# Optimization experiments

Hardware: AMD Instinct MI355X
Metric: run time of the kernel (lower is better)

Reference implementation:

```python
import jax, jax.numpy as jnp
import numpy as np

TAU = 0.5
EPS = 1e-12  # F.normalize default eps


def _projection(z, fc1_w, fc1_b, fc2_w, fc2_b):
    h = jax.nn.elu(z @ fc1_w.T + fc1_b)
    return h @ fc2_w.T + fc2_b


def _normalize(z):
    n = jnp.linalg.norm(z, axis=1, keepdims=True)
    return z / jnp.maximum(n, EPS)


def _semi_loss(h1, h2):
    z1 = _normalize(h1)
    z2 = _normalize(h2)
    refl_sim = jnp.exp((z1 @ z1.T) / TAU)      # [N, N]
    between_sim = jnp.exp((z1 @ z2.T) / TAU)   # [N, N]
    pos = jnp.diagonal(between_sim)
    denom = refl_sim.sum(axis=1) + between_sim.sum(axis=1) - jnp.diagonal(refl_sim)
    return -jnp.log(pos / denom)


def setup_inputs() -> dict:
    key = jax.random.key(0)
    k1, k2, k3, k4 = jax.random.split(key, 4)
    N, H, P = 8192, 512, 512
    s1 = 1.0 / np.sqrt(H)
    s2 = 1.0 / np.sqrt(P)
    return {
        "z1": jax.random.normal(k1, (N, H), jnp.float32),
        "z2": jax.random.normal(k2, (N, H), jnp.float32),
        "fc1_w": jax.random.normal(k3, (P, H), jnp.float32) * s1,
        "fc1_b": jnp.zeros((P,), jnp.float32),
        "fc2_w": jax.random.normal(k4, (H, P), jnp.float32) * s2,
        "fc2_b": jnp.zeros((H,), jnp.float32),
    }


def reference(z1, z2, fc1_w, fc1_b, fc2_w, fc2_b):
    h1 = _projection(z1, fc1_w, fc1_b, fc2_w, fc2_b)
    h2 = _projection(z2, fc1_w, fc1_b, fc2_w, fc2_b)
    l1 = _semi_loss(h1, h2)
    l2 = _semi_loss(h2, h1)
    ret = (l1 + l2) * 0.5
    return ret.mean()
```

## Files before the change

### kernel.cpp

```cpp
#include <hip/hip_runtime.h>
#include <math.h>

typedef __attribute__((ext_vector_type(8))) __bf16 bf16x8;
typedef __attribute__((ext_vector_type(4))) float f32x4;
typedef __attribute__((ext_vector_type(16))) float f32x16;
typedef __attribute__((ext_vector_type(8))) unsigned short u16x8;
typedef __attribute__((ext_vector_type(8))) int i32x8;

#define GAS(p) ((const __attribute__((address_space(1))) void*)(p))
#define LAS(p) ((__attribute__((address_space(3))) void*)(p))

__device__ __forceinline__ unsigned short f2bf(float f) {
  union { float f; unsigned int u; } v; v.f = f;
  unsigned int r = (v.u + 0x7FFFu + ((v.u >> 16) & 1u)) >> 16;
  return (unsigned short)r;
}
__device__ __forceinline__ float bf2f(unsigned short b) {
  union { unsigned int u; float f; } v; v.u = ((unsigned int)b) << 16;
  return v.f;
}

__global__ __launch_bounds__(256) void cast_all_kernel(
    const float* __restrict__ z1, const float* __restrict__ z2,
    const float* __restrict__ w1, const float* __restrict__ w2,
    unsigned short* __restrict__ z1b, unsigned short* __restrict__ z2b,
    unsigned short* __restrict__ w1b, unsigned short* __restrict__ w2b) {
  int b = blockIdx.x;
  const float* in; unsigned short* out; int base;
  if (b < 4096)       { in = z1; out = z1b; base = b; }
  else if (b < 8192)  { in = z2; out = z2b; base = b - 4096; }
  else if (b < 8448)  { in = w1; out = w1b; base = b - 8192; }
  else                { in = w2; out = w2b; base = b - 8448; }
  int i = (base * 256 + threadIdx.x) * 4;
  float4 v = *(const float4*)(in + i);
  ushort4 o;
  o.x = f2bf(v.x); o.y = f2bf(v.y); o.z = f2bf(v.z); o.w = f2bf(v.w);
  *(ushort4*)(out + i) = o;
}

__device__ __forceinline__ void gemm_tile_512(
    const unsigned short* __restrict__ A, const unsigned short* __restrict__ B,
    int m0, int n0, unsigned short* lA, unsigned short* lB, f32x4 acc[4][4]) {
  constexpr int K = 512;
  const int tid  = threadIdx.x;
  const int wave = tid >> 6;
  const int lane = tid & 63;
  const int quad = lane >> 4;
  const int l16  = lane & 15;
  const int wrow = (wave & 1) * 64;
  const int wcol = (wave >> 1) * 64;

  const f32x4 zero = {0.f, 0.f, 0.f, 0.f};
#pragma unroll
  for (int i = 0; i < 4; ++i)
#pragma unroll
    for (int j = 0; j < 4; ++j) acc[i][j] = zero;

  const int e0 = wave * 1024 + lane * 8;
  const int r0 = e0 >> 5, c0 = e0 & 31;
  const int e1 = e0 + 512;
  const int r1 = e1 >> 5, c1 = e1 & 31;

  const unsigned short* Ag0 = A + (size_t)(m0 + r0) * K + c0;
  const unsigned short* Ag1 = A + (size_t)(m0 + r1) * K + c1;
  const unsigned short* Bg0 = B + (size_t)(n0 + r0) * K + c0;
  const unsigned short* Bg1 = B + (size_t)(n0 + r1) * K + c1;

  for (int kt = 0; kt < K; kt += 32) {
    __syncthreads();
    __builtin_amdgcn_global_load_lds(GAS(Ag0 + kt), LAS(&lA[e0]), 16, 0, 0);
    __builtin_amdgcn_global_load_lds(GAS(Ag1 + kt), LAS(&lA[e1]), 16, 0, 0);
    __builtin_amdgcn_global_load_lds(GAS(Bg0 + kt), LAS(&lB[e0]), 16, 0, 0);
    __builtin_amdgcn_global_load_lds(GAS(Bg1 + kt), LAS(&lB[e1]), 16, 0, 0);
    __syncthreads();

    bf16x8 af[4], bfr[4];
#pragma unroll
    for (int i = 0; i < 4; ++i) {
      af[i]  = *(const bf16x8*)&lA[(wrow + i * 16 + l16) * 32 + quad * 8];
      bfr[i] = *(const bf16x8*)&lB[(wcol + i * 16 + l16) * 32 + quad * 8];
    }
#pragma unroll
    for (int mi = 0; mi < 4; ++mi)
#pragma unroll
      for (int ni = 0; ni < 4; ++ni)
        acc[mi][ni] = __builtin_amdgcn_mfma_f32_16x16x32_bf16(
            af[mi], bfr[ni], acc[mi][ni], 0, 0, 0);
  }
}

template<int EPI>
__global__ __launch_bounds__(256)
void proj_kernel(const unsigned short* __restrict__ A1,
                 const unsigned short* __restrict__ A2,
                 const unsigned short* __restrict__ W,
                 const float* __restrict__ bias,
                 unsigned short* __restrict__ C1,
                 unsigned short* __restrict__ C2) {
  __shared__ unsigned short lA[128 * 32];
  __shared__ unsigned short lB[128 * 32];
  const int b = blockIdx.x;
  const int which = b >> 8;
  const int r = b & 255;
  const int n0 = (r & 3) * 128;
  const int m0 = (r >> 2) * 128;
  const unsigned short* A = which ? A2 : A1;
  unsigned short* C = which ? C2 : C1;

  f32x4 acc[4][4];
  gemm_tile_512(A, W, m0, n0, lA, lB, acc);

  const int lane = threadIdx.x & 63;
  const int wave = threadIdx.x >> 6;
  const int quad = lane >> 4;
  const int l16  = lane & 15;
  const int wrow = (wave & 1) * 64;
  const int wcol = (wave >> 1) * 64;

#pragma unroll
  for (int ni = 0; ni < 4; ++ni) {
    const int c = n0 + wcol + ni * 16 + l16;
    const float bv = bias[c];
#pragma unroll
    for (int mi = 0; mi < 4; ++mi) {
      const int rbase = m0 + wrow + mi * 16 + quad * 4;
#pragma unroll
      for (int rr = 0; rr < 4; ++rr) {
        float v = acc[mi][ni][rr] + bv;
        if constexpr (EPI == 0) v = (v > 0.f) ? v : expm1f(v);
        C[(size_t)(rbase + rr) * 512 + c] = f2bf(v);
      }
    }
  }
}

__global__ __launch_bounds__(256, 2)
void gram_kernel(const unsigned char* __restrict__ q1,
                 const unsigned char* __restrict__ q2,
                 float* __restrict__ d11, float* __restrict__ d22,
                 float* __restrict__ d12r, float* __restrict__ d12c) {
  __shared__ unsigned char lA[65536];

  const int b = blockIdx.x;
  const unsigned char *Abase, *Bbase;
  float *rptr, *cptr;
  int by, g, cnt;
  bool cross;
  if (b < 1088) {
    const bool first = (b < 544);
    int j = first ? b : b - 544;
    int q = (int)((sqrtf(2.f * j + 1.f) - 1.f) * 0.5f);
    while (2 * (q + 1) * (q + 2) <= j) ++q;
    while (2 * q * (q + 1) > j) --q;
    const int w = j - 2 * q * (q + 1);
    const int dr = w / (q + 1);
    g = w - dr * (q + 1);
    by = 4 * q + dr;
    const unsigned char* h = first ? q1 : q2;
    Abase = h; Bbase = h;
    rptr = first ? d11 : d22; cptr = rptr;
    cnt = min(4, by + 1 - g * 4);
    cross = false;
  } else {
    const int j = b - 1088;
    g = j >> 6; by = j & 63;
    Abase = q1; Bbase = q2;
    rptr = d12r; cptr = d12c;
    cnt = 4; cross = true;
  }

  const int tid  = threadIdx.x;
  const int wave = tid >> 6;
  const int lane = tid & 63;
  const int half = lane >> 5;
  const int l31  = lane & 31;
  const int pa0 = (wave & 1) * 2;
  const int pb0 = (wave >> 1) * 2;
  const int lfo = half * 1024 + l31 * 16;

  {
    const unsigned char* Asrc = Abase + (size_t)(by * 4 + wave) * 16384 + lane * 16;
    unsigned char* Adst = lA + wave * 16384 + lane * 16;
#pragma unroll
    for (int i = 0; i < 16; ++i)
      __builtin_amdgcn_global_load_lds(GAS(Asrc + i * 1024),
                                       LAS(Adst + i * 1024), 16, 0, 0);
  }
  __syncthreads();

  union frag { i32x8 v; int4 h[2]; };

  float rs[2][16];
#pragma unroll
  for (int mi = 0; mi < 2; ++mi)
#pragma unroll
    for (int rr = 0; rr < 16; ++rr) rs[mi][rr] = 0.f;

  for (int t = 0; t < cnt; ++t) {
    const int ct = g * 4 + t;
    const unsigned char* B0 = Bbase + (size_t)(ct * 4 + pb0) * 16384 + lfo;
    const unsigned char* B1 = B0 + 16384;

    f32x16 acc[2][2];
#pragma unroll
    for (int i = 0; i < 2; ++i)
#pragma unroll
      for (int jj = 0; jj < 2; ++jj)
#pragma unroll
        for (int rr = 0; rr < 16; ++rr) acc[i][jj][rr] = 0.f;

#pragma unroll
    for (int KT = 0; KT < 4; ++KT) {
#pragma unroll
      for (int ktl = 0; ktl < 2; ++ktl) {
        const int ko = KT * 4096 + ktl * 2048;
        frag fa[2], fb[2];
        fb[0].h[0] = *(const int4*)(B0 + ko);
        fb[0].h[1] = *(const int4*)(B0 + ko + 512);
        fb[1].h[0] = *(const int4*)(B1 + ko);
        fb[1].h[1] = *(const int4*)(B1 + ko + 512);
#pragma unroll
        for (int i = 0; i < 2; ++i) {
          const int oa = (pa0 + i) * 16384 + ko + lfo;
          fa[i].h[0] = *(const int4*)&lA[oa];
          fa[i].h[1] = *(const int4*)&lA[oa + 512];
        }
#pragma unroll
        for (int mi = 0; mi < 2; ++mi)
#pragma unroll
          for (int ni = 0; ni < 2; ++ni)
            acc[mi][ni] = __builtin_amdgcn_mfma_scale_f32_32x32x64_f8f6f4(
                fa[mi].v, fb[ni].v, acc[mi][ni],
                0, 0,
                0, 0x7F7F7F7F,
                0, 0x7F7F7F7F);
      }
    }

    float cs[2] = {0.f, 0.f};
#pragma unroll
    for (int mi = 0; mi < 2; ++mi)
#pragma unroll
      for (int ni = 0; ni < 2; ++ni)
#pragma unroll
        for (int rr = 0; rr < 16; ++rr) {
          float v = __expf(2.0f * acc[mi][ni][rr]);
          rs[mi][rr] += v;
          cs[ni] += v;
        }
    const bool diag = (!cross) && (ct == by);
    if (!diag) {
#pragma unroll
      for (int ni = 0; ni < 2; ++ni) {
        float v = cs[ni] + __shfl_xor(cs[ni], 32, 64);
        if (half == 0)
          atomicAdd(&cptr[ct * 128 + (wave >> 1) * 64 + ni * 32 + l31], v);
      }
    }
  }

#pragma unroll
  for (int mi = 0; mi < 2; ++mi) {
#pragma unroll
    for (int d = 1; d < 32; d <<= 1) {
#pragma unroll
      for (int rr = 0; rr < 16; ++rr) rs[mi][rr] += __shfl_xor(rs[mi][rr], d, 64);
    }
    if (l31 == 0) {
      const int mb = by * 128 + (wave & 1) * 64 + mi * 32;
#pragma unroll
      for (int rr = 0; rr < 16; ++rr) {
        const int row = mb + (rr & 3) + 8 * (rr >> 2) + 4 * half;
        atomicAdd(&rptr[row], rs[mi][rr]);
      }
    }
  }
}

__global__ __launch_bounds__(256)
void norm_diag_kernel(const unsigned short* __restrict__ h1,
                      const unsigned short* __restrict__ h2,
                      unsigned char* __restrict__ q1,
                      unsigned char* __restrict__ q2,
                      float* __restrict__ cdiag) {
  const int wave = threadIdx.x >> 6, lane = threadIdx.x & 63;
  const int row = blockIdx.x * 4 + wave;
  const u16x8 u1 = *(const u16x8*)(h1 + (size_t)row * 512 + lane * 8);
  const u16x8 u2 = *(const u16x8*)(h2 + (size_t)row * 512 + lane * 8);
  float f1[8], f2[8], ss1 = 0.f, ss2 = 0.f;
#pragma unroll
  for (int j = 0; j < 8; ++j) {
    f1[j] = bf2f(u1[j]); ss1 += f1[j] * f1[j];
    f2[j] = bf2f(u2[j]); ss2 += f2[j] * f2[j];
  }
#pragma unroll
  for (int d = 1; d < 64; d <<= 1) {
    ss1 += __shfl_xor(ss1, d, 64);
    ss2 += __shfl_xor(ss2, d, 64);
  }
  const float inv1 = 1.0f / fmaxf(sqrtf(ss1), 1e-12f);
  const float inv2 = 1.0f / fmaxf(sqrtf(ss2), 1e-12f);
  float a[8], bb[8];
  float dot = 0.f;
#pragma unroll
  for (int j = 0; j < 8; ++j) {
    a[j] = f1[j] * inv1; bb[j] = f2[j] * inv2;
    dot += a[j] * bb[j];
  }
  int lo1 = __builtin_amdgcn_cvt_pk_fp8_f32(a[0], a[1], 0, false);
  lo1 = __builtin_amdgcn_cvt_pk_fp8_f32(a[2], a[3], lo1, true);
  int hi1 = __builtin_amdgcn_cvt_pk_fp8_f32(a[4], a[5], 0, false);
  hi1 = __builtin_amdgcn_cvt_pk_fp8_f32(a[6], a[7], hi1, true);
  int lo2 = __builtin_amdgcn_cvt_pk_fp8_f32(bb[0], bb[1], 0, false);
  lo2 = __builtin_amdgcn_cvt_pk_fp8_f32(bb[2], bb[3], lo2, true);
  int hi2 = __builtin_amdgcn_cvt_pk_fp8_f32(bb[4], bb[5], 0, false);
  hi2 = __builtin_amdgcn_cvt_pk_fp8_f32(bb[6], bb[7], hi2, true);

  const int c0 = lane * 8;
  const size_t dst = (size_t)(row >> 5) * 16384 + (c0 >> 6) * 2048
                   + ((c0 >> 4) & 3) * 512 + (row & 31) * 16 + (c0 & 15);
  *(int2*)(q1 + dst) = make_int2(lo1, hi1);
  *(int2*)(q2 + dst) = make_int2(lo2, hi2);
#pragma unroll
  for (int d = 1; d < 64; d <<= 1) dot += __shfl_xor(dot, d, 64);
  if (lane == 0) cdiag[row] = dot;
}

__global__ __launch_bounds__(256)
void finalize_kernel(const float* __restrict__ d11, const float* __restrict__ d22,
                     const float* __restrict__ d12r, const float* __restrict__ d12c,
                     const float* __restrict__ cdiag, float* __restrict__ out) {
  const float e2 = 7.38905609893065f;
  float s = 0.f;
  for (int i = threadIdx.x; i < 8192; i += 256) {
    const float den1 = d11[i] + d12r[i] - e2;
    const float den2 = d22[i] + d12c[i] - e2;
    s += -2.0f * cdiag[i] + 0.5f * (logf(den1) + logf(den2));
  }
#pragma unroll
  for (int d = 1; d < 64; d <<= 1) s += __shfl_xor(s, d, 64);
  __shared__ float sm[4];
  if ((threadIdx.x & 63) == 0) sm[threadIdx.x >> 6] = s;
  __syncthreads();
  if (threadIdx.x == 0) out[0] = (sm[0] + sm[1] + sm[2] + sm[3]) * (1.0f / 8192.0f);
}

extern "C" void kernel_launch(void* const* d_in, const int* in_sizes, int n_in,
                              void* d_out, int out_size, void* d_ws, size_t ws_size,
                              hipStream_t stream) {
  const float* z1 = (const float*)d_in[0];
  const float* z2 = (const float*)d_in[1];
  const float* w1 = (const float*)d_in[2];
  const float* b1 = (const float*)d_in[3];
  const float* w2 = (const float*)d_in[4];
  const float* b2 = (const float*)d_in[5];
  float* out = (float*)d_out;

  const int N = 8192, D = 512;
  char* ws = (char*)d_ws;
  auto alloc = [&](size_t bytes) {
    char* p = ws; ws += (bytes + 255) & ~(size_t)255; return p;
  };
  unsigned short* z1b = (unsigned short*)alloc((size_t)N * D * 2);
  unsigned short* z2b = (unsigned short*)alloc((size_t)N * D * 2);
  unsigned short* g1  = (unsigned short*)alloc((size_t)N * D * 2);
  unsigned short* g2  = (unsigned short*)alloc((size_t)N * D * 2);
  unsigned short* w1b = (unsigned short*)alloc((size_t)D * D * 2);
  unsigned short* w2b = (unsigned short*)alloc((size_t)D * D * 2);
  float* sums  = (float*)alloc((size_t)4 * N * sizeof(float));
  float* cdiag = (float*)alloc((size_t)N * sizeof(float));
  float* d11 = sums, *d22 = sums + N, *d12r = sums + 2 * N, *d12c = sums + 3 * N;
  unsigned short* h1 = z1b;
  unsigned short* h2 = z2b;
  unsigned char* q1 = (unsigned char*)g1;
  unsigned char* q2 = (unsigned char*)g2;

  hipMemsetAsync(sums, 0, (size_t)4 * N * sizeof(float), stream);

  cast_all_kernel<<<dim3(8704), 256, 0, stream>>>(z1, z2, w1, w2, z1b, z2b, w1b, w2b);
  proj_kernel<0><<<dim3(512), 256, 0, stream>>>(z1b, z2b, w1b, b1, g1, g2);
  proj_kernel<1><<<dim3(512), 256, 0, stream>>>(g1, g2, w2b, b2, h1, h2);
  norm_diag_kernel<<<dim3(N / 4), 256, 0, stream>>>(h1, h2, q1, q2, cdiag);
  gram_kernel<<<dim3(2112), 256, 0, stream>>>(q1, q2, d11, d22, d12r, d12c);
  finalize_kernel<<<1, 256, 0, stream>>>(d11, d22, d12r, d12c, cdiag, out);
}
```

Baseline: 246.1 us.

## Double-buffer projection GEMM LDS and retile gram kernel to 64-row blocks

The projection GEMM now double-buffers its LDS tiles, issuing the next k-slice's global-to-LDS loads before computing on the current one, with a single barrier per iteration. The gram kernel is retiled so each block holds a 64-row A strip (32 KB LDS) and each wave owns a 64-column slice of a 256-column B supertile. This doubles the number of blocks and raises the occupancy target to 4 blocks per CU. Waves skip sub-diagonal work inside diagonal supertiles, and the exponential is rewritten as exp2 with a folded constant. The risks are more atomics and duplicated B reads, plus the question of whether the single barrier per iteration is enough to order the LDS buffer reuse.

```diff
diff --git a/kernel.cpp b/kernel.cpp
--- a/kernel.cpp
+++ b/kernel.cpp
@@ -38,7 +38,7 @@
   *(ushort4*)(out + i) = o;
 }
 
-__device__ __forceinline__ void gemm_tile_512(
+__device__ __forceinline__ void gemm_tile_512_db(
     const unsigned short* __restrict__ A, const unsigned short* __restrict__ B,
     int m0, int n0, unsigned short* lA, unsigned short* lB, f32x4 acc[4][4]) {
   constexpr int K = 512;
@@ -66,19 +66,27 @@
   const unsigned short* Bg0 = B + (size_t)(n0 + r0) * K + c0;
   const unsigned short* Bg1 = B + (size_t)(n0 + r1) * K + c1;
 
-  for (int kt = 0; kt < K; kt += 32) {
-    __syncthreads();
-    __builtin_amdgcn_global_load_lds(GAS(Ag0 + kt), LAS(&lA[e0]), 16, 0, 0);
-    __builtin_amdgcn_global_load_lds(GAS(Ag1 + kt), LAS(&lA[e1]), 16, 0, 0);
-    __builtin_amdgcn_global_load_lds(GAS(Bg0 + kt), LAS(&lB[e0]), 16, 0, 0);
-    __builtin_amdgcn_global_load_lds(GAS(Bg1 + kt), LAS(&lB[e1]), 16, 0, 0);
-    __syncthreads();
-
+  __builtin_amdgcn_global_load_lds(GAS(Ag0), LAS(&lA[e0]), 16, 0, 0);
+  __builtin_amdgcn_global_load_lds(GAS(Ag1), LAS(&lA[e1]), 16, 0, 0);
+  __builtin_amdgcn_global_load_lds(GAS(Bg0), LAS(&lB[e0]), 16, 0, 0);
+  __builtin_amdgcn_global_load_lds(GAS(Bg1), LAS(&lB[e1]), 16, 0, 0);
+  __syncthreads();
+
+  for (int kt = 0; kt < 16; ++kt) {
+    const int cur = (kt & 1) * 4096;
+    if (kt < 15) {
+      const int nxt = 4096 - cur;
+      const int ko = (kt + 1) * 32;
+      __builtin_amdgcn_global_load_lds(GAS(Ag0 + ko), LAS(&lA[nxt + e0]), 16, 0, 0);
+      __builtin_amdgcn_global_load_lds(GAS(Ag1 + ko), LAS(&lA[nxt + e1]), 16, 0, 0);
+      __builtin_amdgcn_global_load_lds(GAS(Bg0 + ko), LAS(&lB[nxt + e0]), 16, 0, 0);
+      __builtin_amdgcn_global_load_lds(GAS(Bg1 + ko), LAS(&lB[nxt + e1]), 16, 0, 0);
+    }
     bf16x8 af[4], bfr[4];
 #pragma unroll
     for (int i = 0; i < 4; ++i) {
-      af[i]  = *(const bf16x8*)&lA[(wrow + i * 16 + l16) * 32 + quad * 8];
-      bfr[i] = *(const bf16x8*)&lB[(wcol + i * 16 + l16) * 32 + quad * 8];
+      af[i]  = *(const bf16x8*)&lA[cur + (wrow + i * 16 + l16) * 32 + quad * 8];
+      bfr[i] = *(const bf16x8*)&lB[cur + (wcol + i * 16 + l16) * 32 + quad * 8];
     }
 #pragma unroll
     for (int mi = 0; mi < 4; ++mi)
@@ -86,6 +94,7 @@
       for (int ni = 0; ni < 4; ++ni)
         acc[mi][ni] = __builtin_amdgcn_mfma_f32_16x16x32_bf16(
             af[mi], bfr[ni], acc[mi][ni], 0, 0, 0);
+    __syncthreads();
   }
 }
 
@@ -97,8 +106,8 @@
                  const float* __restrict__ bias,
                  unsigned short* __restrict__ C1,
                  unsigned short* __restrict__ C2) {
-  __shared__ unsigned short lA[128 * 32];
-  __shared__ unsigned short lB[128 * 32];
+  __shared__ unsigned short lA[2 * 128 * 32];
+  __shared__ unsigned short lB[2 * 128 * 32];
   const int b = blockIdx.x;
   const int which = b >> 8;
   const int r = b & 255;
@@ -108,7 +117,7 @@
   unsigned short* C = which ? C2 : C1;
 
   f32x4 acc[4][4];
-  gemm_tile_512(A, W, m0, n0, lA, lB, acc);
+  gemm_tile_512_db(A, W, m0, n0, lA, lB, acc);
 
   const int lane = threadIdx.x & 63;
   const int wave = threadIdx.x >> 6;
@@ -134,39 +143,39 @@
   }
 }
 
-__global__ __launch_bounds__(256, 2)
+__global__ __launch_bounds__(256, 4)
 void gram_kernel(const unsigned char* __restrict__ q1,
                  const unsigned char* __restrict__ q2,
                  float* __restrict__ d11, float* __restrict__ d22,
                  float* __restrict__ d12r, float* __restrict__ d12c) {
-  __shared__ unsigned char lA[65536];
+  __shared__ unsigned char lA[32768];
 
   const int b = blockIdx.x;
   const unsigned char *Abase, *Bbase;
   float *rptr, *cptr;
-  int by, g, cnt;
+  int r, g, cnt;
   bool cross;
-  if (b < 1088) {
-    const bool first = (b < 544);
-    int j = first ? b : b - 544;
-    int q = (int)((sqrtf(2.f * j + 1.f) - 1.f) * 0.5f);
-    while (2 * (q + 1) * (q + 2) <= j) ++q;
-    while (2 * q * (q + 1) > j) --q;
-    const int w = j - 2 * q * (q + 1);
-    const int dr = w / (q + 1);
-    g = w - dr * (q + 1);
-    by = 4 * q + dr;
+  if (b < 2176) {
+    const bool first = (b < 1088);
+    int j = first ? b : b - 1088;
+    int q = (int)((sqrtf((float)j + 1.f) - 1.f) * 0.5f);
+    while (4 * (q + 1) * (q + 2) <= j) ++q;
+    while (4 * q * (q + 1) > j) --q;
+    const int w = j - 4 * q * (q + 1);
+    const int s = w / (q + 1);
+    g = w - s * (q + 1);
+    r = 8 * q + s;
     const unsigned char* h = first ? q1 : q2;
     Abase = h; Bbase = h;
     rptr = first ? d11 : d22; cptr = rptr;
-    cnt = min(4, by + 1 - g * 4);
+    cnt = min(2, (r >> 2) + 1 - 2 * g);
     cross = false;
   } else {
-    const int j = b - 1088;
-    g = j >> 6; by = j & 63;
+    const int j = b - 2176;
+    g = j >> 7; r = j & 127;
     Abase = q1; Bbase = q2;
     rptr = d12r; cptr = d12c;
-    cnt = 4; cross = true;
+    cnt = 2; cross = true;
   }
 
   const int tid  = threadIdx.x;
@@ -174,15 +183,13 @@
   const int lane = tid & 63;
   const int half = lane >> 5;
   const int l31  = lane & 31;
-  const int pa0 = (wave & 1) * 2;
-  const int pb0 = (wave >> 1) * 2;
-  const int lfo = half * 1024 + l31 * 16;
+  const int lfo  = half * 1024 + l31 * 16;
 
   {
-    const unsigned char* Asrc = Abase + (size_t)(by * 4 + wave) * 16384 + lane * 16;
-    unsigned char* Adst = lA + wave * 16384 + lane * 16;
-#pragma unroll
-    for (int i = 0; i < 16; ++i)
+    const unsigned char* Asrc = Abase + (size_t)r * 32768 + wave * 8192 + lane * 16;
+    unsigned char* Adst = lA + wave * 8192 + lane * 16;
+#pragma unroll
+    for (int i = 0; i < 8; ++i)
       __builtin_amdgcn_global_load_lds(GAS(Asrc + i * 1024),
                                        LAS(Adst + i * 1024), 16, 0, 0);
   }
@@ -196,9 +203,12 @@
 #pragma unroll
     for (int rr = 0; rr < 16; ++rr) rs[mi][rr] = 0.f;
 
+  const int d = r & 3;
   for (int t = 0; t < cnt; ++t) {
-    const int ct = g * 4 + t;
-    const unsigned char* B0 = Bbase + (size_t)(ct * 4 + pb0) * 16384 + lfo;
+    const int c = 2 * g + t;
+    const bool diagST = (!cross) && (c == (r >> 2));
+    if (diagST && wave > d) break;
+    const unsigned char* B0 = Bbase + (size_t)(8 * c + 2 * wave) * 16384 + lfo;
     const unsigned char* B1 = B0 + 16384;
 
     f32x16 acc[2][2];
@@ -221,7 +231,7 @@
         fb[1].h[1] = *(const int4*)(B1 + ko + 512);
 #pragma unroll
         for (int i = 0; i < 2; ++i) {
-          const int oa = (pa0 + i) * 16384 + ko + lfo;
+          const int oa = i * 16384 + ko + lfo;
           fa[i].h[0] = *(const int4*)&lA[oa];
           fa[i].h[1] = *(const int4*)&lA[oa + 512];
         }
@@ -244,17 +254,16 @@
       for (int ni = 0; ni < 2; ++ni)
 #pragma unroll
         for (int rr = 0; rr < 16; ++rr) {
-          float v = __expf(2.0f * acc[mi][ni][rr]);
+          float v = exp2f(2.8853900817779268f * acc[mi][ni][rr]);
           rs[mi][rr] += v;
           cs[ni] += v;
         }
-    const bool diag = (!cross) && (ct == by);
-    if (!diag) {
+    if (!(diagST && wave == d)) {
 #pragma unroll
       for (int ni = 0; ni < 2; ++ni) {
         float v = cs[ni] + __shfl_xor(cs[ni], 32, 64);
         if (half == 0)
-          atomicAdd(&cptr[ct * 128 + (wave >> 1) * 64 + ni * 32 + l31], v);
+          atomicAdd(&cptr[c * 256 + wave * 64 + ni * 32 + l31], v);
       }
     }
   }
@@ -262,12 +271,12 @@
 #pragma unroll
   for (int mi = 0; mi < 2; ++mi) {
 #pragma unroll
-    for (int d = 1; d < 32; d <<= 1) {
-#pragma unroll
-      for (int rr = 0; rr < 16; ++rr) rs[mi][rr] += __shfl_xor(rs[mi][rr], d, 64);
+    for (int dd = 1; dd < 32; dd <<= 1) {
+#pragma unroll
+      for (int rr = 0; rr < 16; ++rr) rs[mi][rr] += __shfl_xor(rs[mi][rr], dd, 64);
     }
     if (l31 == 0) {
-      const int mb = by * 128 + (wave & 1) * 64 + mi * 32;
+      const int mb = r * 64 + mi * 32;
 #pragma unroll
       for (int rr = 0; rr < 16; ++rr) {
         const int row = mb + (rr & 3) + 8 * (rr >> 2) + 4 * half;
@@ -381,6 +390,6 @@
   proj_kernel<0><<<dim3(512), 256, 0, stream>>>(z1b, z2b, w1b, b1, g1, g2);
   proj_kernel<1><<<dim3(512), 256, 0, stream>>>(g1, g2, w2b, b2, h1, h2);
   norm_diag_kernel<<<dim3(N / 4), 256, 0, stream>>>(h1, h2, q1, q2, cdiag);
-  gram_kernel<<<dim3(2112), 256, 0, stream>>>(q1, q2, d11, d22, d12r, d12c);
+  gram_kernel<<<dim3(4224), 256, 0, stream>>>(q1, q2, d11, d22, d12r, d12c);
   finalize_kernel<<<1, 256, 0, stream>>>(d11, d22, d12r, d12c, cdiag, out);
 }
```

Result: slower. 299.6 us (+21.7%).

## Double-buffer projection GEMM LDS tiles and prefetch B fragments in sim kernel

Applied to the files above, without the earlier changes.

The projection GEMM now double-buffers its LDS tiles: the loads for the next K-slice are issued before computing on the current one, and one barrier per iteration replaces two. The similarity kernel keeps a 4-deep ring of B-fragment registers and prefetches two K-steps ahead, crossing into the next column tile, so global load latency overlaps the MFMA work. The exp is rewritten as exp2f with a prescaled constant. The cost is double the LDS in the projection kernel and more registers in the sim kernel, which may reduce occupancy.

```diff
diff --git a/kernel.cpp b/kernel.cpp
--- a/kernel.cpp
+++ b/kernel.cpp
@@ -38,7 +38,7 @@
   *(ushort4*)(out + i) = o;
 }
 
-__device__ __forceinline__ void gemm_tile_512(
+__device__ __forceinline__ void gemm_tile_512_db(
     const unsigned short* __restrict__ A, const unsigned short* __restrict__ B,
     int m0, int n0, unsigned short* lA, unsigned short* lB, f32x4 acc[4][4]) {
   constexpr int K = 512;
@@ -66,19 +66,27 @@
   const unsigned short* Bg0 = B + (size_t)(n0 + r0) * K + c0;
   const unsigned short* Bg1 = B + (size_t)(n0 + r1) * K + c1;
 
-  for (int kt = 0; kt < K; kt += 32) {
-    __syncthreads();
-    __builtin_amdgcn_global_load_lds(GAS(Ag0 + kt), LAS(&lA[e0]), 16, 0, 0);
-    __builtin_amdgcn_global_load_lds(GAS(Ag1 + kt), LAS(&lA[e1]), 16, 0, 0);
-    __builtin_amdgcn_global_load_lds(GAS(Bg0 + kt), LAS(&lB[e0]), 16, 0, 0);
-    __builtin_amdgcn_global_load_lds(GAS(Bg1 + kt), LAS(&lB[e1]), 16, 0, 0);
-    __syncthreads();
-
+  __builtin_amdgcn_global_load_lds(GAS(Ag0), LAS(&lA[e0]), 16, 0, 0);
+  __builtin_amdgcn_global_load_lds(GAS(Ag1), LAS(&lA[e1]), 16, 0, 0);
+  __builtin_amdgcn_global_load_lds(GAS(Bg0), LAS(&lB[e0]), 16, 0, 0);
+  __builtin_amdgcn_global_load_lds(GAS(Bg1), LAS(&lB[e1]), 16, 0, 0);
+  __syncthreads();
+
+  for (int kt = 0; kt < 16; ++kt) {
+    const int cur = (kt & 1) * 4096;
+    if (kt < 15) {
+      const int nxt = 4096 - cur;
+      const int ko = (kt + 1) * 32;
+      __builtin_amdgcn_global_load_lds(GAS(Ag0 + ko), LAS(&lA[nxt + e0]), 16, 0, 0);
+      __builtin_amdgcn_global_load_lds(GAS(Ag1 + ko), LAS(&lA[nxt + e1]), 16, 0, 0);
+      __builtin_amdgcn_global_load_lds(GAS(Bg0 + ko), LAS(&lB[nxt + e0]), 16, 0, 0);
+      __builtin_amdgcn_global_load_lds(GAS(Bg1 + ko), LAS(&lB[nxt + e1]), 16, 0, 0);
+    }
     bf16x8 af[4], bfr[4];
 #pragma unroll
     for (int i = 0; i < 4; ++i) {
-      af[i]  = *(const bf16x8*)&lA[(wrow + i * 16 + l16) * 32 + quad * 8];
-      bfr[i] = *(const bf16x8*)&lB[(wcol + i * 16 + l16) * 32 + quad * 8];
+      af[i]  = *(const bf16x8*)&lA[cur + (wrow + i * 16 + l16) * 32 + quad * 8];
+      bfr[i] = *(const bf16x8*)&lB[cur + (wcol + i * 16 + l16) * 32 + quad * 8];
     }
 #pragma unroll
     for (int mi = 0; mi < 4; ++mi)
@@ -86,6 +94,7 @@
       for (int ni = 0; ni < 4; ++ni)
         acc[mi][ni] = __builtin_amdgcn_mfma_f32_16x16x32_bf16(
             af[mi], bfr[ni], acc[mi][ni], 0, 0, 0);
+    __syncthreads();
   }
 }
 
@@ -97,8 +106,8 @@
                  const float* __restrict__ bias,
                  unsigned short* __restrict__ C1,
                  unsigned short* __restrict__ C2) {
-  __shared__ unsigned short lA[128 * 32];
-  __shared__ unsigned short lB[128 * 32];
+  __shared__ unsigned short lA[2 * 128 * 32];
+  __shared__ unsigned short lB[2 * 128 * 32];
   const int b = blockIdx.x;
   const int which = b >> 8;
   const int r = b & 255;
@@ -108,7 +117,7 @@
   unsigned short* C = which ? C2 : C1;
 
   f32x4 acc[4][4];
-  gemm_tile_512(A, W, m0, n0, lA, lB, acc);
+  gemm_tile_512_db(A, W, m0, n0, lA, lB, acc);
 
   const int lane = threadIdx.x & 63;
   const int wave = threadIdx.x >> 6;
@@ -190,16 +199,30 @@
 
   union frag { i32x8 v; int4 h[2]; };
 
+  auto LDB = [&](frag* dst, const unsigned char* base, int uu) {
+    const int off = (uu >> 1) * 4096 + (uu & 1) * 2048;
+    dst[0].h[0] = *(const int4*)(base + off);
+    dst[0].h[1] = *(const int4*)(base + off + 512);
+    dst[1].h[0] = *(const int4*)(base + 16384 + off);
+    dst[1].h[1] = *(const int4*)(base + 16384 + off + 512);
+  };
+
   float rs[2][16];
 #pragma unroll
   for (int mi = 0; mi < 2; ++mi)
 #pragma unroll
     for (int rr = 0; rr < 16; ++rr) rs[mi][rr] = 0.f;
+
+  frag fb[4][2];
+  const unsigned char* curB =
+      Bbase + (size_t)(g * 4 * 4 + pb0) * 16384 + lfo;
+  LDB(fb[0], curB, 0);
+  LDB(fb[1], curB, 1);
 
   for (int t = 0; t < cnt; ++t) {
     const int ct = g * 4 + t;
-    const unsigned char* B0 = Bbase + (size_t)(ct * 4 + pb0) * 16384 + lfo;
-    const unsigned char* B1 = B0 + 16384;
+    const unsigned char* nxtB = curB + 4 * 16384;
+    const bool hasNext = (t + 1 < cnt);
 
     f32x16 acc[2][2];
 #pragma unroll
@@ -210,31 +233,27 @@
         for (int rr = 0; rr < 16; ++rr) acc[i][jj][rr] = 0.f;
 
 #pragma unroll
-    for (int KT = 0; KT < 4; ++KT) {
-#pragma unroll
-      for (int ktl = 0; ktl < 2; ++ktl) {
-        const int ko = KT * 4096 + ktl * 2048;
-        frag fa[2], fb[2];
-        fb[0].h[0] = *(const int4*)(B0 + ko);
-        fb[0].h[1] = *(const int4*)(B0 + ko + 512);
-        fb[1].h[0] = *(const int4*)(B1 + ko);
-        fb[1].h[1] = *(const int4*)(B1 + ko + 512);
-#pragma unroll
-        for (int i = 0; i < 2; ++i) {
-          const int oa = (pa0 + i) * 16384 + ko + lfo;
-          fa[i].h[0] = *(const int4*)&lA[oa];
-          fa[i].h[1] = *(const int4*)&lA[oa + 512];
-        }
-#pragma unroll
-        for (int mi = 0; mi < 2; ++mi)
-#pragma unroll
-          for (int ni = 0; ni < 2; ++ni)
-            acc[mi][ni] = __builtin_amdgcn_mfma_scale_f32_32x32x64_f8f6f4(
-                fa[mi].v, fb[ni].v, acc[mi][ni],
-                0, 0,
-                0, 0x7F7F7F7F,
-                0, 0x7F7F7F7F);
+    for (int u = 0; u < 8; ++u) {
+      if (u < 6)            LDB(fb[(u + 2) & 3], curB, u + 2);
+      else if (hasNext)     LDB(fb[(u + 2) & 3], nxtB, u - 6);
+
+      const int ko = (u >> 1) * 4096 + (u & 1) * 2048;
+      frag fa[2];
+#pragma unroll
+      for (int i = 0; i < 2; ++i) {
+        const int oa = (pa0 + i) * 16384 + ko + lfo;
+        fa[i].h[0] = *(const int4*)&lA[oa];
+        fa[i].h[1] = *(const int4*)&lA[oa + 512];
       }
+#pragma unroll
+      for (int mi = 0; mi < 2; ++mi)
+#pragma unroll
+        for (int ni = 0; ni < 2; ++ni)
+          acc[mi][ni] = __builtin_amdgcn_mfma_scale_f32_32x32x64_f8f6f4(
+              fa[mi].v, fb[u & 3][ni].v, acc[mi][ni],
+              0, 0,
+              0, 0x7F7F7F7F,
+              0, 0x7F7F7F7F);
     }
 
     float cs[2] = {0.f, 0.f};
@@ -244,7 +263,7 @@
       for (int ni = 0; ni < 2; ++ni)
 #pragma unroll
         for (int rr = 0; rr < 16; ++rr) {
-          float v = __expf(2.0f * acc[mi][ni][rr]);
+          float v = exp2f(2.8853900817779268f * acc[mi][ni][rr]);
           rs[mi][rr] += v;
           cs[ni] += v;
         }
@@ -257,14 +276,15 @@
           atomicAdd(&cptr[ct * 128 + (wave >> 1) * 64 + ni * 32 + l31], v);
       }
     }
+    curB = nxtB;
   }
 
 #pragma unroll
   for (int mi = 0; mi < 2; ++mi) {
 #pragma unroll
-    for (int d = 1; d < 32; d <<= 1) {
-#pragma unroll
-      for (int rr = 0; rr < 16; ++rr) rs[mi][rr] += __shfl_xor(rs[mi][rr], d, 64);
+    for (int dd = 1; dd < 32; dd <<= 1) {
+#pragma unroll
+      for (int rr = 0; rr < 16; ++rr) rs[mi][rr] += __shfl_xor(rs[mi][rr], dd, 64);
     }
     if (l31 == 0) {
       const int mb = by * 128 + (wave & 1) * 64 + mi * 32;
```

Result: slower. 472.4 us (+91.9%).
